# Kernel optimization log

Measured on AMD Instinct MI355X. Metric: run time of the kernel, lower is better.

Reference implementation:

```python
import jax, jax.numpy as jnp
import numpy as np

DEG_U = 3
DEG_V = 3
EPS = 1e-6


def uniform_knot_vectors(n_cp, degree, n_surf, n_fac):
    # first `degree` zeros, linspace(0,1) over the middle, last `degree` ones
    interior = jnp.linspace(0.0, 1.0, n_cp + degree + 1 - 2 * degree, dtype=jnp.float32)
    kv = jnp.concatenate([jnp.zeros(degree, jnp.float32), interior, jnp.ones(degree, jnp.float32)])
    return jnp.broadcast_to(kv, (n_surf, n_fac, kv.shape[0]))


def find_spans_uniform(u, n_cp, degree):
    # uniform clamped knot vector: n_unique = n_cp - degree + 1 distinct knots
    n_unique = n_cp - degree + 1
    return jnp.floor(u * (n_unique - 1)).astype(jnp.int32) + degree


def basis_funs_and_derivs(u, span, knots, p, n=1):
    """NURBS Book A2.3, vectorized over [S,F,P]. Returns ders[k][j] arrays."""
    def kn(off):
        return jnp.take_along_axis(knots, span + off, axis=2)

    left = [None] * (p + 1)
    right = [None] * (p + 1)
    ndu = [[None] * (p + 1) for _ in range(p + 1)]
    ndu[0][0] = jnp.ones_like(u)
    for j in range(1, p + 1):
        left[j] = u - kn(1 - j)
        right[j] = kn(j) - u
        saved = jnp.zeros_like(u)
        for r in range(j):
            ndu[j][r] = right[r + 1] + left[j - r]
            temp = ndu[r][j - 1] / ndu[j][r]
            ndu[r][j] = saved + right[r + 1] * temp
            saved = left[j - r] * temp
        ndu[j][j] = saved

    ders = [[None] * (p + 1) for _ in range(n + 1)]
    for j in range(p + 1):
        ders[0][j] = ndu[j][p]
    for r in range(p + 1):
        s1, s2 = 0, 1
        a = [[jnp.zeros_like(u) for _ in range(p + 1)] for _ in range(2)]
        a[0][0] = jnp.ones_like(u)
        for k in range(1, n + 1):
            d = jnp.zeros_like(u)
            rk, pk = r - k, p - k
            if r >= k:
                a[s2][0] = a[s1][0] / ndu[pk + 1][rk]
                d = a[s2][0] * ndu[rk][pk]
            j1 = 1 if rk >= -1 else -rk
            j2 = k - 1 if r - 1 <= pk else p - r
            for jj in range(j1, j2 + 1):
                a[s2][jj] = (a[s1][jj] - a[s1][jj - 1]) / ndu[pk + 1][rk + jj]
                d = d + a[s2][jj] * ndu[rk + jj][pk]
            if r <= pk:
                a[s2][k] = -a[s1][k - 1] / ndu[pk + 1][r]
                d = d + a[s2][k] * ndu[r][pk]
            ders[k][r] = d
            s1, s2 = s2, s1
    fac = float(p)
    for k in range(1, n + 1):
        for j in range(p + 1):
            ders[k][j] = ders[k][j] * fac
        fac *= p - k
    return ders


def setup_inputs() -> dict:
    key = jax.random.key(0)
    k1, k2 = jax.random.split(key)
    S, F, P = 8, 4, 200000
    Ncu, Ncv = 32, 32
    evaluation_points = jax.random.uniform(k1, (S, F, P, 2), dtype=jnp.float32) * (1.0 - EPS)
    control_points = jax.random.normal(k2, (S, F, Ncu, Ncv, 3), dtype=jnp.float32)
    return {"evaluation_points": evaluation_points, "control_points": control_points}


def reference(evaluation_points, control_points):
    S, F, Ncu, Ncv, _ = control_points.shape
    u = evaluation_points[..., 0]  # [S,F,P]
    v = evaluation_points[..., 1]
    knots_u = uniform_knot_vectors(Ncu, DEG_U, S, F)
    knots_v = uniform_knot_vectors(Ncv, DEG_V, S, F)
    span_u = find_spans_uniform(u, Ncu, DEG_U)
    span_v = find_spans_uniform(v, Ncv, DEG_V)
    du_basis = basis_funs_and_derivs(u, span_u, knots_u, DEG_U, 1)
    dv_basis = basis_funs_and_derivs(v, span_v, knots_v, DEG_V, 1)

    bs = jnp.arange(S)[:, None, None]
    bf = jnp.arange(F)[None, :, None]
    pt = 0.0
    d_u = 0.0
    d_v = 0.0
    for i in range(DEG_U + 1):
        iu = span_u - DEG_U + i  # [S,F,P]
        Nu0 = du_basis[0][i][..., None]
        Nu1 = du_basis[1][i][..., None]
        for j in range(DEG_V + 1):
            iv = span_v - DEG_V + j
            cpij = control_points[bs, bf, iu, iv]  # [S,F,P,3]
            Nv0 = dv_basis[0][j][..., None]
            Nv1 = dv_basis[1][j][..., None]
            pt = pt + Nu0 * Nv0 * cpij
            d_u = d_u + Nu1 * Nv0 * cpij
            d_v = d_v + Nu0 * Nv1 * cpij
    normals = jnp.cross(d_u, d_v)
    normals = normals / (jnp.linalg.norm(normals, axis=-1, keepdims=True) + 1e-12)
    return pt, normals
```

## Files before the change

kernel.cpp:

```cpp
#include <hip/hip_runtime.h>


#define NCP 32
#define KMAX 29

__device__ __forceinline__ float rcp29(int d) {
    return (d == 1) ? 29.0f : ((d == 2) ? 14.5f : (29.0f / 3.0f));
}

__device__ __forceinline__ void basis3(float u, int a, float B0[4], float B1[4]) {
    const float s = 1.0f / 29.0f;
    float km2 = (float)max(a - 2, 0) * s;
    float km1 = (float)max(a - 1, 0) * s;
    float k00 = (float)a * s;
    float kp1 = (float)(a + 1) * s;
    float kp2 = (float)min(a + 2, KMAX) * s;
    float kp3 = (float)min(a + 3, KMAX) * s;
    float l1 = u - k00, l2 = u - km1, l3 = u - km2;
    float r1 = kp1 - u, r2 = kp2 - u, r3 = kp3 - u;
    float q20 = rcp29(min(a + 1, 2));
    float q21 = rcp29(min(KMAX - a, 2));
    float q30 = rcp29(min(a + 1, 3));
    float q31 = rcp29(min(min(a + 2, 30 - a), 3));
    float q32 = rcp29(min(KMAX - a, 3));
    float n01 = r1 * 29.0f;
    float n11 = l1 * 29.0f;
    float t = n01 * q20;
    float n02 = r1 * t;
    float sv = l2 * t;
    t = n11 * q21;
    float n12 = fmaf(r2, t, sv);
    float n22 = l1 * t;
    float t0 = n02 * q30;
    B0[0] = r1 * t0;
    sv = l3 * t0;
    float t1 = n12 * q31;
    B0[1] = fmaf(r2, t1, sv);
    sv = l2 * t1;
    float t2 = n22 * q32;
    B0[2] = fmaf(r3, t2, sv);
    B0[3] = l1 * t2;
    B1[0] = -3.0f * t0;
    B1[1] = 3.0f * (t0 - t1);
    B1[2] = 3.0f * (t1 - t2);
    B1[3] = 3.0f * t2;
}

__global__ __launch_bounds__(1024, 8) void nurbs_eval_kernel(
    const float2* __restrict__ ev,
    const float*  __restrict__ cp,
    float* __restrict__ out_pt,
    float* __restrict__ out_nrm,
    int P)
{
    __shared__ float4 win[NCP * NCP * 3];

    const int sf = blockIdx.y;
    const float* g = cp + (size_t)sf * (NCP * NCP * 3);
    for (int idx = threadIdx.x; idx < NCP * 29; idx += blockDim.x) {
        int row = idx / 29;
        int c   = idx - row * 29;
        const float* r = g + (row * NCP + c) * 3;
        float x0 = r[0], y0 = r[1],  z0 = r[2];
        float x1 = r[3], y1 = r[4],  z1 = r[5];
        float x2 = r[6], y2 = r[7],  z2 = r[8];
        float x3 = r[9], y3 = r[10], z3 = r[11];
        int w = (row * NCP + c) * 3;
        win[w + 0] = make_float4(x0, y0, z0, x1);
        win[w + 1] = make_float4(y1, z1, x2, y2);
        win[w + 2] = make_float4(z2, x3, y3, z3);
    }
    __syncthreads();

    const int p = blockIdx.x * blockDim.x + threadIdx.x;
    if (p >= P) return;
    const int t = sf * P + p;

    float2 uv = ev[t];
    int au = min((int)(uv.x * 29.0f), 28);
    int av = min((int)(uv.y * 29.0f), 28);

    float B0u[4], B1u[4], B0v[4], B1v[4];
    basis3(uv.x, au, B0u, B1u);
    basis3(uv.y, av, B0v, B1v);
    const float bv0 = B0v[0], bv1 = B0v[1], bv2 = B0v[2], bv3 = B0v[3];
    const float dv0 = B1v[0], dv1 = B1v[1], dv2 = B1v[2], dv3 = B1v[3];

    float px = 0.f, py = 0.f, pz = 0.f;
    float ux = 0.f, uy = 0.f, uz = 0.f;
    float vx = 0.f, vy = 0.f, vz = 0.f;
    const int base = (au * NCP + av) * 3;
#pragma unroll
    for (int i = 0; i < 4; ++i) {
        const float4 q0 = win[base + i * (NCP * 3) + 0];
        const float4 q1 = win[base + i * (NCP * 3) + 1];
        const float4 q2 = win[base + i * (NCP * 3) + 2];
        const float cx0 = q0.x, cy0 = q0.y, cz0 = q0.z;
        const float cx1 = q0.w, cy1 = q1.x, cz1 = q1.y;
        const float cx2 = q1.z, cy2 = q1.w, cz2 = q2.x;
        const float cx3 = q2.y, cy3 = q2.z, cz3 = q2.w;
        float rpx = fmaf(bv3, cx3, fmaf(bv2, cx2, fmaf(bv1, cx1, bv0 * cx0)));
        float rpy = fmaf(bv3, cy3, fmaf(bv2, cy2, fmaf(bv1, cy1, bv0 * cy0)));
        float rpz = fmaf(bv3, cz3, fmaf(bv2, cz2, fmaf(bv1, cz1, bv0 * cz0)));
        float rvx = fmaf(dv3, cx3, fmaf(dv2, cx2, fmaf(dv1, cx1, dv0 * cx0)));
        float rvy = fmaf(dv3, cy3, fmaf(dv2, cy2, fmaf(dv1, cy1, dv0 * cy0)));
        float rvz = fmaf(dv3, cz3, fmaf(dv2, cz2, fmaf(dv1, cz1, dv0 * cz0)));
        const float bu = B0u[i], du = B1u[i];
        px = fmaf(bu, rpx, px); py = fmaf(bu, rpy, py); pz = fmaf(bu, rpz, pz);
        ux = fmaf(du, rpx, ux); uy = fmaf(du, rpy, uy); uz = fmaf(du, rpz, uz);
        vx = fmaf(bu, rvx, vx); vy = fmaf(bu, rvy, vy); vz = fmaf(bu, rvz, vz);
    }

    float nx = uy * vz - uz * vy;
    float ny = uz * vx - ux * vz;
    float nz = ux * vy - uy * vx;
    float d   = fmaf(nx, nx, fmaf(ny, ny, nz * nz));
    float len = __builtin_amdgcn_sqrtf(d);
    float inv = __builtin_amdgcn_rcpf(len + 1e-12f);
    nx *= inv; ny *= inv; nz *= inv;

    const int o = t * 3;
    out_pt[o + 0] = px;
    out_pt[o + 1] = py;
    out_pt[o + 2] = pz;
    out_nrm[o + 0] = nx;
    out_nrm[o + 1] = ny;
    out_nrm[o + 2] = nz;
}

extern "C" void kernel_launch(void* const* d_in, const int* in_sizes, int n_in,
                              void* d_out, int out_size, void* d_ws, size_t ws_size,
                              hipStream_t stream) {
    (void)n_in; (void)d_ws; (void)ws_size; (void)out_size;
    const int SF = in_sizes[1] / (NCP * NCP * 3);
    const int P  = in_sizes[0] / (SF * 2);
    const int N  = SF * P;

    const float2* ev = (const float2*)d_in[0];
    const float*  cp = (const float*)d_in[1];
    float* out_pt  = (float*)d_out;
    float* out_nrm = (float*)d_out + (size_t)N * 3;

    dim3 block(1024);
    dim3 grid((P + 1023) / 1024, SF);
    nurbs_eval_kernel<<<grid, block, 0, stream>>>(ev, cp, out_pt, out_nrm, P);
}
```

Measured before the change: 209.6 us.

## Process two points per thread with vectorized I/O and simplified normalized basis

Each thread now evaluates two consecutive points. It loads their parameters as one float4 and writes outputs as float2 pairs, and block size is halved to 512 so the shared control-point window is loaded once per twice as much work. The basis computation is rewritten in span-normalized coordinates (U*29), which drops the knot divisions and the 29 scale factors; the derivative scale of 29 and 3 cancels, a normalization-invariant step because only normals use derivatives. This assumes P is even and the buffer is aligned for float4 and float2 access, and span clamping at u=1 is no longer applied explicitly.

```diff
diff --git a/kernel.cpp b/kernel.cpp
--- a/kernel.cpp
+++ b/kernel.cpp
@@ -2,52 +2,47 @@
 
 
 #define NCP 32
-#define KMAX 29
 
-__device__ __forceinline__ float rcp29(int d) {
-    return (d == 1) ? 29.0f : ((d == 2) ? 14.5f : (29.0f / 3.0f));
+__device__ __forceinline__ void basis3u(float U, float B0[4], float B1[4], int& A)
+{
+    float Af = floorf(U);
+    A = (int)Af;
+    float t  = U - Af;
+    float c1 = fminf(Af, 1.0f);
+    float c2 = fminf(Af, 2.0f);
+    float gg = 29.0f - Af;
+    float e1 = fminf(gg, 2.0f);
+    float e2 = fminf(gg, 3.0f);
+    float L1 = t, L2 = t + c1, L3 = t + c2;
+    float R1 = 1.0f - t, R2 = e1 - t, R3 = e2 - t;
+    float q20 = (Af < 1.0f) ? 1.0f : 0.5f;
+    float q21 = (gg < 2.0f) ? 1.0f : 0.5f;
+    float q30 = (Af < 1.0f) ? 1.0f : ((Af < 2.0f) ? 0.5f : (1.0f / 3.0f));
+    float q31 = ((Af < 1.0f) || (gg < 2.0f)) ? 0.5f : (1.0f / 3.0f);
+    float q32 = (gg < 2.0f) ? 1.0f : ((gg < 3.0f) ? 0.5f : (1.0f / 3.0f));
+    float ta  = R1 * q20;
+    float n02 = R1 * ta;
+    float sv  = L2 * ta;
+    float tb  = L1 * q21;
+    float n12 = fmaf(R2, tb, sv);
+    float n22 = L1 * tb;
+    float t0 = n02 * q30;
+    B0[0] = R1 * t0;
+    sv = L3 * t0;
+    float t1 = n12 * q31;
+    B0[1] = fmaf(R2, t1, sv);
+    sv = L2 * t1;
+    float t2 = n22 * q32;
+    B0[2] = fmaf(R3, t2, sv);
+    B0[3] = L1 * t2;
+    B1[0] = -t0;
+    B1[1] = t0 - t1;
+    B1[2] = t1 - t2;
+    B1[3] = t2;
 }
 
-__device__ __forceinline__ void basis3(float u, int a, float B0[4], float B1[4]) {
-    const float s = 1.0f / 29.0f;
-    float km2 = (float)max(a - 2, 0) * s;
-    float km1 = (float)max(a - 1, 0) * s;
-    float k00 = (float)a * s;
-    float kp1 = (float)(a + 1) * s;
-    float kp2 = (float)min(a + 2, KMAX) * s;
-    float kp3 = (float)min(a + 3, KMAX) * s;
-    float l1 = u - k00, l2 = u - km1, l3 = u - km2;
-    float r1 = kp1 - u, r2 = kp2 - u, r3 = kp3 - u;
-    float q20 = rcp29(min(a + 1, 2));
-    float q21 = rcp29(min(KMAX - a, 2));
-    float q30 = rcp29(min(a + 1, 3));
-    float q31 = rcp29(min(min(a + 2, 30 - a), 3));
-    float q32 = rcp29(min(KMAX - a, 3));
-    float n01 = r1 * 29.0f;
-    float n11 = l1 * 29.0f;
-    float t = n01 * q20;
-    float n02 = r1 * t;
-    float sv = l2 * t;
-    t = n11 * q21;
-    float n12 = fmaf(r2, t, sv);
-    float n22 = l1 * t;
-    float t0 = n02 * q30;
-    B0[0] = r1 * t0;
-    sv = l3 * t0;
-    float t1 = n12 * q31;
-    B0[1] = fmaf(r2, t1, sv);
-    sv = l2 * t1;
-    float t2 = n22 * q32;
-    B0[2] = fmaf(r3, t2, sv);
-    B0[3] = l1 * t2;
-    B1[0] = -3.0f * t0;
-    B1[1] = 3.0f * (t0 - t1);
-    B1[2] = 3.0f * (t1 - t2);
-    B1[3] = 3.0f * t2;
-}
-
-__global__ __launch_bounds__(1024, 8) void nurbs_eval_kernel(
-    const float2* __restrict__ ev,
+__global__ __launch_bounds__(512, 6) void nurbs_eval_kernel(
+    const float4* __restrict__ ev4,
     const float*  __restrict__ cp,
     float* __restrict__ out_pt,
     float* __restrict__ out_nrm,
@@ -57,75 +52,78 @@
 
     const int sf = blockIdx.y;
     const float* g = cp + (size_t)sf * (NCP * NCP * 3);
-    for (int idx = threadIdx.x; idx < NCP * 29; idx += blockDim.x) {
+    for (int idx = threadIdx.x; idx < NCP * 29; idx += 512) {
         int row = idx / 29;
         int c   = idx - row * 29;
         const float* r = g + (row * NCP + c) * 3;
-        float x0 = r[0], y0 = r[1],  z0 = r[2];
-        float x1 = r[3], y1 = r[4],  z1 = r[5];
-        float x2 = r[6], y2 = r[7],  z2 = r[8];
-        float x3 = r[9], y3 = r[10], z3 = r[11];
         int w = (row * NCP + c) * 3;
-        win[w + 0] = make_float4(x0, y0, z0, x1);
-        win[w + 1] = make_float4(y1, z1, x2, y2);
-        win[w + 2] = make_float4(z2, x3, y3, z3);
+        win[w + 0] = make_float4(r[0], r[1], r[2],  r[3]);
+        win[w + 1] = make_float4(r[4], r[5], r[6],  r[7]);
+        win[w + 2] = make_float4(r[8], r[9], r[10], r[11]);
     }
     __syncthreads();
 
-    const int p = blockIdx.x * blockDim.x + threadIdx.x;
-    if (p >= P) return;
-    const int t = sf * P + p;
+    const int p2 = (blockIdx.x * 512 + threadIdx.x) * 2;
+    if (p2 >= P) return;
+    const int t2 = sf * P + p2;
 
-    float2 uv = ev[t];
-    int au = min((int)(uv.x * 29.0f), 28);
-    int av = min((int)(uv.y * 29.0f), 28);
+    const float4 uv = ev4[t2 >> 1];
 
-    float B0u[4], B1u[4], B0v[4], B1v[4];
-    basis3(uv.x, au, B0u, B1u);
-    basis3(uv.y, av, B0v, B1v);
-    const float bv0 = B0v[0], bv1 = B0v[1], bv2 = B0v[2], bv3 = B0v[3];
-    const float dv0 = B1v[0], dv1 = B1v[1], dv2 = B1v[2], dv3 = B1v[3];
+    float pr[2][3], nr[2][3];
+#pragma unroll
+    for (int k = 0; k < 2; ++k) {
+        const float u = k ? uv.z : uv.x;
+        const float v = k ? uv.w : uv.y;
+        int au, av;
+        float B0u[4], B1u[4], B0v[4], B1v[4];
+        basis3u(u * 29.0f, B0u, B1u, au);
+        basis3u(v * 29.0f, B0v, B1v, av);
+        const float bv0 = B0v[0], bv1 = B0v[1], bv2 = B0v[2], bv3 = B0v[3];
+        const float dv0 = B1v[0], dv1 = B1v[1], dv2 = B1v[2], dv3 = B1v[3];
 
-    float px = 0.f, py = 0.f, pz = 0.f;
-    float ux = 0.f, uy = 0.f, uz = 0.f;
-    float vx = 0.f, vy = 0.f, vz = 0.f;
-    const int base = (au * NCP + av) * 3;
+        float px = 0.f, py = 0.f, pz = 0.f;
+        float ux = 0.f, uy = 0.f, uz = 0.f;
+        float vx = 0.f, vy = 0.f, vz = 0.f;
+        const int base = (au * NCP + av) * 3;
 #pragma unroll
-    for (int i = 0; i < 4; ++i) {
-        const float4 q0 = win[base + i * (NCP * 3) + 0];
-        const float4 q1 = win[base + i * (NCP * 3) + 1];
-        const float4 q2 = win[base + i * (NCP * 3) + 2];
-        const float cx0 = q0.x, cy0 = q0.y, cz0 = q0.z;
-        const float cx1 = q0.w, cy1 = q1.x, cz1 = q1.y;
-        const float cx2 = q1.z, cy2 = q1.w, cz2 = q2.x;
-        const float cx3 = q2.y, cy3 = q2.z, cz3 = q2.w;
-        float rpx = fmaf(bv3, cx3, fmaf(bv2, cx2, fmaf(bv1, cx1, bv0 * cx0)));
-        float rpy = fmaf(bv3, cy3, fmaf(bv2, cy2, fmaf(bv1, cy1, bv0 * cy0)));
-        float rpz = fmaf(bv3, cz3, fmaf(bv2, cz2, fmaf(bv1, cz1, bv0 * cz0)));
-        float rvx = fmaf(dv3, cx3, fmaf(dv2, cx2, fmaf(dv1, cx1, dv0 * cx0)));
-        float rvy = fmaf(dv3, cy3, fmaf(dv2, cy2, fmaf(dv1, cy1, dv0 * cy0)));
-        float rvz = fmaf(dv3, cz3, fmaf(dv2, cz2, fmaf(dv1, cz1, dv0 * cz0)));
-        const float bu = B0u[i], du = B1u[i];
-        px = fmaf(bu, rpx, px); py = fmaf(bu, rpy, py); pz = fmaf(bu, rpz, pz);
-        ux = fmaf(du, rpx, ux); uy = fmaf(du, rpy, uy); uz = fmaf(du, rpz, uz);
-        vx = fmaf(bu, rvx, vx); vy = fmaf(bu, rvy, vy); vz = fmaf(bu, rvz, vz);
+        for (int i = 0; i < 4; ++i) {
+            const float4 q0 = win[base + i * (NCP * 3) + 0];
+            const float4 q1 = win[base + i * (NCP * 3) + 1];
+            const float4 q2 = win[base + i * (NCP * 3) + 2];
+            const float cx0 = q0.x, cy0 = q0.y, cz0 = q0.z;
+            const float cx1 = q0.w, cy1 = q1.x, cz1 = q1.y;
+            const float cx2 = q1.z, cy2 = q1.w, cz2 = q2.x;
+            const float cx3 = q2.y, cy3 = q2.z, cz3 = q2.w;
+            float rpx = fmaf(bv3, cx3, fmaf(bv2, cx2, fmaf(bv1, cx1, bv0 * cx0)));
+            float rpy = fmaf(bv3, cy3, fmaf(bv2, cy2, fmaf(bv1, cy1, bv0 * cy0)));
+            float rpz = fmaf(bv3, cz3, fmaf(bv2, cz2, fmaf(bv1, cz1, bv0 * cz0)));
+            float rvx = fmaf(dv3, cx3, fmaf(dv2, cx2, fmaf(dv1, cx1, dv0 * cx0)));
+            float rvy = fmaf(dv3, cy3, fmaf(dv2, cy2, fmaf(dv1, cy1, dv0 * cy0)));
+            float rvz = fmaf(dv3, cz3, fmaf(dv2, cz2, fmaf(dv1, cz1, dv0 * cz0)));
+            const float bu = B0u[i], du = B1u[i];
+            px = fmaf(bu, rpx, px); py = fmaf(bu, rpy, py); pz = fmaf(bu, rpz, pz);
+            ux = fmaf(du, rpx, ux); uy = fmaf(du, rpy, uy); uz = fmaf(du, rpz, uz);
+            vx = fmaf(bu, rvx, vx); vy = fmaf(bu, rvy, vy); vz = fmaf(bu, rvz, vz);
+        }
+
+        float nx = uy * vz - uz * vy;
+        float ny = uz * vx - ux * vz;
+        float nz = ux * vy - uy * vx;
+        float d   = fmaf(nx, nx, fmaf(ny, ny, nz * nz));
+        float len = __builtin_amdgcn_sqrtf(d);
+        float inv = __builtin_amdgcn_rcpf(len + 1e-12f);
+        pr[k][0] = px; pr[k][1] = py; pr[k][2] = pz;
+        nr[k][0] = nx * inv; nr[k][1] = ny * inv; nr[k][2] = nz * inv;
     }
 
-    float nx = uy * vz - uz * vy;
-    float ny = uz * vx - ux * vz;
-    float nz = ux * vy - uy * vx;
-    float d   = fmaf(nx, nx, fmaf(ny, ny, nz * nz));
-    float len = __builtin_amdgcn_sqrtf(d);
-    float inv = __builtin_amdgcn_rcpf(len + 1e-12f);
-    nx *= inv; ny *= inv; nz *= inv;
-
-    const int o = t * 3;
-    out_pt[o + 0] = px;
-    out_pt[o + 1] = py;
-    out_pt[o + 2] = pz;
-    out_nrm[o + 0] = nx;
-    out_nrm[o + 1] = ny;
-    out_nrm[o + 2] = nz;
+    float2* op = (float2*)(out_pt + (size_t)t2 * 3);
+    op[0] = make_float2(pr[0][0], pr[0][1]);
+    op[1] = make_float2(pr[0][2], pr[1][0]);
+    op[2] = make_float2(pr[1][1], pr[1][2]);
+    float2* on = (float2*)(out_nrm + (size_t)t2 * 3);
+    on[0] = make_float2(nr[0][0], nr[0][1]);
+    on[1] = make_float2(nr[0][2], nr[1][0]);
+    on[2] = make_float2(nr[1][1], nr[1][2]);
 }
 
 extern "C" void kernel_launch(void* const* d_in, const int* in_sizes, int n_in,
@@ -136,12 +134,12 @@
     const int P  = in_sizes[0] / (SF * 2);
     const int N  = SF * P;
 
-    const float2* ev = (const float2*)d_in[0];
-    const float*  cp = (const float*)d_in[1];
+    const float4* ev4 = (const float4*)d_in[0];
+    const float*  cp  = (const float*)d_in[1];
     float* out_pt  = (float*)d_out;
     float* out_nrm = (float*)d_out + (size_t)N * 3;
 
-    dim3 block(1024);
+    dim3 block(512);
     dim3 grid((P + 1023) / 1024, SF);
-    nurbs_eval_kernel<<<grid, block, 0, stream>>>(ev, cp, out_pt, out_nrm, P);
+    nurbs_eval_kernel<<<grid, block, 0, stream>>>(ev4, cp, out_pt, out_nrm, P);
 }
```

After: 678.5 us. 3.24x slower.
